# Kernel tuning notes

Hardware: AMD Instinct MI355X
Metric: run time of the kernel (lower is better)

## Reference

```python
import jax, jax.numpy as jnp
import numpy as np

B, N, M, K, D, DO = 4, 32768, 8192, 16, 128, 128


def setup_inputs() -> dict:
    key = jax.random.key(0)
    ks = jax.random.split(key, 8)
    return dict(
        xyz=jax.random.normal(ks[0], (B, N, 3), jnp.float32),
        x=jax.random.normal(ks[1], (B, D, N), jnp.float32),
        xyz_center=jax.random.normal(ks[2], (B, M, 3), jnp.float32),
        idx=jax.random.randint(ks[3], (B, M, K), 0, N, jnp.int32),
        alpha=jnp.ones((1,), jnp.float32),
        beta=jnp.ones((1,), jnp.float32),
        norm_radius=jnp.ones((1,), jnp.float32),
        w1=jax.random.normal(ks[4], (K, 3), jnp.float32) * 0.1,
        g1=jnp.ones((K,), jnp.float32),
        b1=jnp.zeros((K,), jnp.float32),
        w2=jax.random.normal(ks[5], (K, 2 * K), jnp.float32) * 0.1,
        g2=jnp.ones((K,), jnp.float32),
        b2=jnp.zeros((K,), jnp.float32),
        w3=jax.random.normal(ks[6], (K, 2 * K), jnp.float32) * 0.1,
        cv_w=jax.random.normal(ks[7], (DO, D, K), jnp.float32) * 0.02,
    )


def _inorm(t, g, b, eps=1e-5):
    # InstanceNorm2d: normalize each (batch, channel) plane over spatial dims (m, k)
    mu = t.mean(axis=(2, 3), keepdims=True)
    var = t.var(axis=(2, 3), keepdims=True)
    return (t - mu) * jax.lax.rsqrt(var + eps) * g[None, :, None, None] + b[None, :, None, None]


def reference(xyz, x, xyz_center, idx, alpha, beta, norm_radius, w1, g1, b1, w2, g2, b2, w3, cv_w):
    k = idx.shape[-1]
    gather = jax.vmap(lambda pts, i: pts[i])  # per-batch gather
    xyz_group = gather(xyz, idx)                      # b m k 3
    x_group = gather(jnp.swapaxes(x, 1, 2), idx)      # b m k d

    pts = xyz_group - xyz_center[:, :, None, :]       # b m k 3
    # dist computed on detached pts (torch .detach())
    dist = jnp.sqrt(jnp.sum(jnp.square(jax.lax.stop_gradient(pts)), -1))  # b m k
    mean_radius = dist.max(-1).mean()
    nr = norm_radius * 0.9 + mean_radius * 0.1        # EMA-updated radius (non-trainable)
    pts = pts / nr

    dw = jax.nn.sigmoid(-alpha * dist + beta)         # b m k
    s = dw.sum(-1, keepdims=True)
    s = s + (s == 0).astype(dw.dtype) + 1e-6
    dw = dw / s * k
    dw4 = dw[:, None, :, :]                           # b 1 m k

    ptsT = jnp.transpose(pts, (0, 3, 1, 2))           # b 3 m k
    mat = jax.nn.relu(_inorm(jnp.einsum('bcmk,oc->bomk', ptsT, w1), g1, b1))
    mp1 = jnp.broadcast_to((mat * dw4).max(-1, keepdims=True), mat.shape)
    mat = jax.nn.relu(_inorm(jnp.einsum('bcmk,oc->bomk', jnp.concatenate([mat, mp1], 1), w2), g2, b2))
    mp2 = jnp.broadcast_to((mat * dw4).max(-1, keepdims=True), mat.shape)
    mat = jax.nn.relu(jnp.einsum('bcmk,oc->bomk', jnp.concatenate([mat, mp2], 1), w3)) * dw4

    out = jnp.einsum('bmkd,bjmk->bdmj', x_group, mat)  # b d m k
    out = jnp.einsum('bdmj,odj->bom', out, cv_w)
    return out
```

## Files before the change

### kernel.cpp

```cpp
#include <hip/hip_runtime.h>
#include <hip/hip_bf16.h>

#define BB 4
#define NN 32768
#define MM 8192
#define KK 16
#define DD 128
#define DOUT 128
#define TT 2048

typedef unsigned short ushortT;
typedef unsigned int uintT;
typedef __attribute__((ext_vector_type(8))) short short8;
typedef __attribute__((ext_vector_type(4))) float f32x4;
typedef __attribute__((ext_vector_type(2))) float f32x2;

__device__ __forceinline__ ushortT f2bf(float f) {
  union { float f; uintT u; } v; v.f = f;
  uintT u = v.u;
  return (ushortT)((u + 0x7FFFu + ((u >> 16) & 1u)) >> 16);
}

#define ST_MAXD 0
#define ST_E1 16
#define ST_A1 160
#define ST_B1 224
#define ST_E2 288
#define ST_A2 416
#define ST_B2 480

__global__ __launch_bounds__(256) void kxT(const float* __restrict__ x, ushortT* __restrict__ xTb) {
  __shared__ float tile[32][33];
  const int b = blockIdx.z;
  const int n0 = blockIdx.x * 32, d0 = blockIdx.y * 32;
  const int tx = threadIdx.x, ty = threadIdx.y;
  const float* xp = x + (size_t)b * DD * NN;
  #pragma unroll
  for (int i = 0; i < 4; i++)
    tile[ty + i * 8][tx] = xp[(size_t)(d0 + ty + i * 8) * NN + n0 + tx];
  __syncthreads();
  ushortT* op = xTb + (size_t)b * NN * DD;
  #pragma unroll
  for (int i = 0; i < 4; i++)
    op[(size_t)(n0 + ty + i * 8) * DD + d0 + tx] = f2bf(tile[tx][ty + i * 8]);
}

__global__ __launch_bounds__(256) void kWb(const float* __restrict__ cw, ushortT* __restrict__ wb) {
  const int i = blockIdx.x * 256 + threadIdx.x;
  wb[i] = f2bf(cw[i]);
}

__global__ __launch_bounds__(256) void kpassA(const float* __restrict__ xyz,
    const float* __restrict__ xyzc, const int* __restrict__ idx,
    const float* __restrict__ w1, float* __restrict__ st, float4* __restrict__ pts4) {
  const int b = blockIdx.y;
  const int tid = threadIdx.x;
  const int mloc = tid >> 4, k = tid & 15;
  const int m = blockIdx.x * 16 + mloc;
  const int gi = (b * MM + m) * KK + k;
  const int n = idx[gi];
  const float cx = xyzc[(b * MM + m) * 3 + 0];
  const float cy = xyzc[(b * MM + m) * 3 + 1];
  const float cz = xyzc[(b * MM + m) * 3 + 2];
  const float* p = xyz + ((size_t)b * NN + n) * 3;
  const float px = p[0] - cx, py = p[1] - cy, pz = p[2] - cz;
  const float dist = sqrtf(px * px + py * py + pz * pz);
  pts4[gi] = (float4){px, py, pz, dist};
  float maxd = dist;
  maxd = fmaxf(maxd, __shfl_xor(maxd, 1));
  maxd = fmaxf(maxd, __shfl_xor(maxd, 2));
  maxd = fmaxf(maxd, __shfl_xor(maxd, 4));
  maxd = fmaxf(maxd, __shfl_xor(maxd, 8));
  __shared__ float red[16];
  __shared__ float wred[4][32];
  if (k == 0) red[mloc] = maxd;
  float vs[16], vq[16];
  #pragma unroll
  for (int o = 0; o < 16; o++) {
    float e = px * w1[3 * o] + py * w1[3 * o + 1] + pz * w1[3 * o + 2];
    vs[o] = e; vq[o] = e * e;
  }
  #pragma unroll
  for (int s = 1; s < 64; s <<= 1) {
    #pragma unroll
    for (int o = 0; o < 16; o++) {
      vs[o] += __shfl_xor(vs[o], s);
      vq[o] += __shfl_xor(vq[o], s);
    }
  }
  const int wv = tid >> 6, lane = tid & 63;
  if (lane == 0) {
    #pragma unroll
    for (int o = 0; o < 16; o++) { wred[wv][o] = vs[o]; wred[wv][16 + o] = vq[o]; }
  }
  __syncthreads();
  if (tid < 32) {
    float a = wred[0][tid] + wred[1][tid] + wred[2][tid] + wred[3][tid];
    atomicAdd(&st[ST_E1 + b * 32 + tid], a);
  }
  if (tid == 0) {
    float s = 0.f;
    #pragma unroll
    for (int i = 0; i < 16; i++) s += red[i];
    atomicAdd(&st[ST_MAXD], s);
  }
}

__global__ void kS1(const float* __restrict__ nrad, const float* __restrict__ g1,
                    const float* __restrict__ b1, float* __restrict__ st) {
  const int tid = threadIdx.x;
  if (tid >= 64) return;
  const float meanrad = st[ST_MAXD] / (float)(BB * MM);
  const float nr = nrad[0] * 0.9f + meanrad * 0.1f;
  const int b = tid >> 4, o = tid & 15;
  const float cnt = (float)(MM * KK);
  const float sum = st[ST_E1 + b * 32 + o];
  const float sq  = st[ST_E1 + b * 32 + 16 + o];
  const float mu = sum / cnt;
  float var = sq / cnt - mu * mu; var = fmaxf(var, 0.f);
  const float invs = rsqrtf(var + 1e-5f * nr * nr);
  const float a = invs * g1[o];
  st[ST_A1 + b * 16 + o] = a;
  st[ST_B1 + b * 16 + o] = b1[o] - mu * a;
}

__global__ __launch_bounds__(256) void kpassB(const float4* __restrict__ pts4,
    const float* __restrict__ alpha, const float* __restrict__ beta,
    const float* __restrict__ w1, const float* __restrict__ w2,
    float* __restrict__ st) {
  const int b = blockIdx.y;
  const int tid = threadIdx.x;
  __shared__ float w2s[512];
  __shared__ float wred[4][32];
  w2s[tid] = w2[tid]; w2s[256 + tid] = w2[256 + tid];
  const int gi = b * MM * KK + blockIdx.x * 256 + tid;
  const float4 p4 = pts4[gi];
  const float px = p4.x, py = p4.y, pz = p4.z, dist = p4.w;
  float dwv = 1.f / (1.f + expf(alpha[0] * dist - beta[0]));
  float s = dwv;
  s += __shfl_xor(s, 1); s += __shfl_xor(s, 2); s += __shfl_xor(s, 4); s += __shfl_xor(s, 8);
  s = s + (s == 0.f ? 1.f : 0.f) + 1e-6f;
  dwv = dwv / s * 16.f;
  float mat1[16], mp1[16];
  #pragma unroll
  for (int o = 0; o < 16; o++) {
    float e = px * w1[3 * o] + py * w1[3 * o + 1] + pz * w1[3 * o + 2];
    float v = e * st[ST_A1 + b * 16 + o] + st[ST_B1 + b * 16 + o];
    mat1[o] = fmaxf(v, 0.f);
    float t = mat1[o] * dwv;
    t = fmaxf(t, __shfl_xor(t, 1)); t = fmaxf(t, __shfl_xor(t, 2));
    t = fmaxf(t, __shfl_xor(t, 4)); t = fmaxf(t, __shfl_xor(t, 8));
    mp1[o] = t;
  }
  __syncthreads();
  float vs[16], vq[16];
  #pragma unroll
  for (int o = 0; o < 16; o++) {
    float acc = 0.f;
    #pragma unroll
    for (int c = 0; c < 16; c++)
      acc += mat1[c] * w2s[o * 32 + c] + mp1[c] * w2s[o * 32 + 16 + c];
    vs[o] = acc; vq[o] = acc * acc;
  }
  #pragma unroll
  for (int s2 = 1; s2 < 64; s2 <<= 1) {
    #pragma unroll
    for (int o = 0; o < 16; o++) {
      vs[o] += __shfl_xor(vs[o], s2);
      vq[o] += __shfl_xor(vq[o], s2);
    }
  }
  const int wv = tid >> 6, lane = tid & 63;
  if (lane == 0) {
    #pragma unroll
    for (int o = 0; o < 16; o++) { wred[wv][o] = vs[o]; wred[wv][16 + o] = vq[o]; }
  }
  __syncthreads();
  if (tid < 32) {
    float a = wred[0][tid] + wred[1][tid] + wred[2][tid] + wred[3][tid];
    atomicAdd(&st[ST_E2 + b * 32 + tid], a);
  }
}

__global__ void kS2(const float* __restrict__ g2, const float* __restrict__ b2,
                    float* __restrict__ st) {
  const int tid = threadIdx.x;
  if (tid >= 64) return;
  const int b = tid >> 4, o = tid & 15;
  const float cnt = (float)(MM * KK);
  const float sum = st[ST_E2 + b * 32 + o];
  const float sq  = st[ST_E2 + b * 32 + 16 + o];
  const float mu = sum / cnt;
  float var = sq / cnt - mu * mu; var = fmaxf(var, 0.f);
  const float invs = rsqrtf(var + 1e-5f);
  const float a = invs * g2[o];
  st[ST_A2 + b * 16 + o] = a;
  st[ST_B2 + b * 16 + o] = b2[o] - mu * a;
}

__global__ __launch_bounds__(512, 4) void kF1(const float4* __restrict__ pts4,
    const int* __restrict__ idx,
    const float* __restrict__ alpha, const float* __restrict__ beta,
    const float* __restrict__ w1, const float* __restrict__ w2, const float* __restrict__ w3,
    const float* __restrict__ st, const ushortT* __restrict__ xTb, ushortT* __restrict__ Aout) {
  __shared__ float w2s[512], w3s[512];
  __shared__ float mat3s[32 * 256];
  __shared__ ushortT nls[512];
  const int b = blockIdx.y;
  const int tid = threadIdx.x;
  const int m0 = blockIdx.x * 32;
  w2s[tid] = w2[tid];
  w3s[tid] = w3[tid];

  const int mloc = tid >> 4, k1 = tid & 15;
  const int gi = (b * MM + m0) * KK + tid;
  nls[tid] = (ushortT)idx[gi];
  const float4 p4 = pts4[gi];
  const float px = p4.x, py = p4.y, pz = p4.z, dist = p4.w;
  float dwv = 1.f / (1.f + expf(alpha[0] * dist - beta[0]));
  {
    float s = dwv;
    s += __shfl_xor(s, 1); s += __shfl_xor(s, 2); s += __shfl_xor(s, 4); s += __shfl_xor(s, 8);
    s = s + (s == 0.f ? 1.f : 0.f) + 1e-6f;
    dwv = dwv / s * 16.f;
  }
  float mat1[16], mp1[16];
  #pragma unroll
  for (int o = 0; o < 16; o++) {
    float e = px * w1[3 * o] + py * w1[3 * o + 1] + pz * w1[3 * o + 2];
    float v = e * st[ST_A1 + b * 16 + o] + st[ST_B1 + b * 16 + o];
    mat1[o] = fmaxf(v, 0.f);
    float t = mat1[o] * dwv;
    t = fmaxf(t, __shfl_xor(t, 1)); t = fmaxf(t, __shfl_xor(t, 2));
    t = fmaxf(t, __shfl_xor(t, 4)); t = fmaxf(t, __shfl_xor(t, 8));
    mp1[o] = t;
  }
  __syncthreads();
  {
    float mat2[16], mp2[16];
    #pragma unroll
    for (int o = 0; o < 16; o++) {
      float acc = 0.f;
      #pragma unroll
      for (int c = 0; c < 16; c++)
        acc += mat1[c] * w2s[o * 32 + c] + mp1[c] * w2s[o * 32 + 16 + c];
      float v = acc * st[ST_A2 + b * 16 + o] + st[ST_B2 + b * 16 + o];
      mat2[o] = fmaxf(v, 0.f);
      float t = mat2[o] * dwv;
      t = fmaxf(t, __shfl_xor(t, 1)); t = fmaxf(t, __shfl_xor(t, 2));
      t = fmaxf(t, __shfl_xor(t, 4)); t = fmaxf(t, __shfl_xor(t, 8));
      mp2[o] = t;
    }
    const int swz1 = (k1 ^ (k1 >> 2)) & 3;
    float* m3w = &mat3s[mloc * 256 + k1 * 16];
    float m3v[16];
    #pragma unroll
    for (int j = 0; j < 16; j++) {
      float acc = 0.f;
      #pragma unroll
      for (int c = 0; c < 16; c++)
        acc += mat2[c] * w3s[j * 32 + c] + mp2[c] * w3s[j * 32 + 16 + c];
      m3v[j] = fmaxf(acc, 0.f) * dwv;
    }
    #pragma unroll
    for (int q = 0; q < 4; q++)
      *(f32x4*)(m3w + ((q ^ swz1) << 2)) =
          (f32x4){m3v[4 * q], m3v[4 * q + 1], m3v[4 * q + 2], m3v[4 * q + 3]};
  }
  __syncthreads();

  const int wid = tid >> 6;
  const int lane = tid & 63;
  const int jh = lane >> 5;
  const int dq = lane & 31;
  const int d0 = dq * 4;
  const int jq0 = jh * 2;
  const ushortT* xb = xTb + (size_t)b * NN * DD + d0;

  uint2 xA[16], xB[16];

#define PREF(dst, gg) do {                                                 \
    const ushortT* nb = &nls[((gg) * 8 + wid) * 16];                       \
    _Pragma("unroll")                                                      \
    for (int k = 0; k < 16; k++) {                                         \
      const uintT nn = nb[k];                                              \
      (dst)[k] = *(const uint2*)(xb + ((size_t)nn << 7));                  \
    }                                                                      \
  } while (0)

#define COMP(src, gg) do {                                                 \
    const int ml = (gg) * 8 + wid;                                         \
    const float* m3base = &mat3s[ml * 256];                                \
    f32x2 a2[4][4];                                                        \
    _Pragma("unroll")                                                      \
    for (int d = 0; d < 4; d++)                                            \
      _Pragma("unroll")                                                    \
      for (int c = 0; c < 4; c++) a2[d][c] = (f32x2){0.f, 0.f};            \
    _Pragma("unroll")                                                      \
    for (int k = 0; k < 16; k++) {                                         \
      const int sw = (k ^ (k >> 2)) & 3;                                   \
      const uint2 xv = (src)[k];                                           \
      const f32x4 mq0 = *(const f32x4*)(m3base + k * 16 + ((jq0 ^ sw) << 2));        \
      const f32x4 mq1 = *(const f32x4*)(m3base + k * 16 + (((jq0 + 1) ^ sw) << 2));  \
      float xs[4];                                                         \
      xs[0] = __uint_as_float(xv.x << 16);                                 \
      xs[1] = __uint_as_float(xv.x & 0xFFFF0000u);                         \
      xs[2] = __uint_as_float(xv.y << 16);                                 \
      xs[3] = __uint_as_float(xv.y & 0xFFFF0000u);                         \
      f32x2 mp[4];                                                         \
      mp[0] = mq0.lo; mp[1] = mq0.hi;                                      \
      mp[2] = mq1.lo; mp[3] = mq1.hi;                                      \
      _Pragma("unroll")                                                    \
      for (int d = 0; d < 4; d++) {                                        \
        const float xd = xs[d];                                            \
        _Pragma("unroll")                                                  \
        for (int c = 0; c < 4; c++)                                        \
          a2[d][c] += mp[c] * xd;                                          \
      }                                                                    \
    }                                                                      \
    ushortT* aop = Aout + ((size_t)b * MM + m0 + ml) * TT + d0 * 16 + jh * 8;  \
    _Pragma("unroll")                                                      \
    for (int d = 0; d < 4; d++) {                                          \
      uintT u[4];                                                          \
      _Pragma("unroll")                                                    \
      for (int c = 0; c < 4; c++)                                          \
        u[c] = (uintT)f2bf(a2[d][c].x) | ((uintT)f2bf(a2[d][c].y) << 16);  \
      *(uint4*)(aop + d * 16) = (uint4){u[0], u[1], u[2], u[3]};           \
    }                                                                      \
  } while (0)

  PREF(xA, 0);
  PREF(xB, 1);
  COMP(xA, 0);
  PREF(xA, 2);
  COMP(xB, 1);
  PREF(xB, 3);
  COMP(xA, 2);
  COMP(xB, 3);

#undef PREF
#undef COMP
}

__global__ __launch_bounds__(512) void kgemm(const ushortT* __restrict__ Wb,
                                             const ushortT* __restrict__ Aout,
                                             float* __restrict__ out) {
  __shared__ ushortT At[128 * 40];
  __shared__ ushortT Bt[128 * 40];
  const int b = blockIdx.y;
  const int m0 = blockIdx.x * 128;
  const int tid = threadIdx.x;
  const int w = tid >> 6, l = tid & 63;
  const int ow = (w >> 2) * 64, mw = (w & 3) * 32;
  const int fr = l & 15, fg = l >> 4;
  f32x4 acc[4][2];
  #pragma unroll
  for (int i = 0; i < 4; i++)
    #pragma unroll
    for (int j = 0; j < 2; j++)
      acc[i][j] = (f32x4){0.f, 0.f, 0.f, 0.f};
  const int srow = tid >> 2, sk = (tid & 3) * 8;
  const ushortT* wp = Wb + srow * TT + sk;
  const ushortT* ap = Aout + ((size_t)b * MM + m0 + srow) * TT + sk;
  for (int k0 = 0; k0 < TT; k0 += 32) {
    uint4 wv = *(const uint4*)(wp + k0);
    uint4 av = *(const uint4*)(ap + k0);
    *(uint4*)&At[srow * 40 + sk] = wv;
    *(uint4*)&Bt[srow * 40 + sk] = av;
    __syncthreads();
    short8 a[4], bfrag[2];
    #pragma unroll
    for (int i = 0; i < 4; i++) a[i] = *(short8*)&At[(ow + i * 16 + fr) * 40 + fg * 8];
    #pragma unroll
    for (int j = 0; j < 2; j++) bfrag[j] = *(short8*)&Bt[(mw + j * 16 + fr) * 40 + fg * 8];
    #pragma unroll
    for (int i = 0; i < 4; i++)
      #pragma unroll
      for (int j = 0; j < 2; j++)
        acc[i][j] = __builtin_amdgcn_mfma_f32_16x16x32_bf16(a[i], bfrag[j], acc[i][j], 0, 0, 0);
    __syncthreads();
  }
  #pragma unroll
  for (int i = 0; i < 4; i++)
    #pragma unroll
    for (int j = 0; j < 2; j++)
      #pragma unroll
      for (int r = 0; r < 4; r++) {
        const int o = ow + i * 16 + fg * 4 + r;
        const int m = m0 + mw + j * 16 + fr;
        out[((size_t)b * DOUT + o) * MM + m] = acc[i][j][r];
      }
}

#define XTB_OFF 0
#define PTS_OFF 33554432
#define AOUT_OFF 67108864
#define WB_OFF 201326592
#define ST_OFF 201850880

extern "C" void kernel_launch(void* const* d_in, const int* in_sizes, int n_in,
                              void* d_out, int out_size, void* d_ws, size_t ws_size,
                              hipStream_t stream) {
  const float* xyz  = (const float*)d_in[0];
  const float* x    = (const float*)d_in[1];
  const float* xyzc = (const float*)d_in[2];
  const int*   idx  = (const int*)d_in[3];
  const float* alpha = (const float*)d_in[4];
  const float* beta  = (const float*)d_in[5];
  const float* nrad  = (const float*)d_in[6];
  const float* w1 = (const float*)d_in[7];
  const float* g1 = (const float*)d_in[8];
  const float* b1 = (const float*)d_in[9];
  const float* w2 = (const float*)d_in[10];
  const float* g2 = (const float*)d_in[11];
  const float* b2 = (const float*)d_in[12];
  const float* w3 = (const float*)d_in[13];
  const float* cvw = (const float*)d_in[14];
  char* ws = (char*)d_ws;
  ushortT* xTb  = (ushortT*)(ws + XTB_OFF);
  float4*  pts4 = (float4*)(ws + PTS_OFF);
  ushortT* Aout = (ushortT*)(ws + AOUT_OFF);
  ushortT* Wb   = (ushortT*)(ws + WB_OFF);
  float*   st   = (float*)(ws + ST_OFF);
  float* out = (float*)d_out;

  hipMemsetAsync(st, 0, 4096, stream);
  kxT<<<dim3(NN / 32, DD / 32, BB), dim3(32, 8), 0, stream>>>(x, xTb);
  kWb<<<dim3(DOUT * TT / 256), 256, 0, stream>>>(cvw, Wb);
  kpassA<<<dim3(MM / 16, BB), 256, 0, stream>>>(xyz, xyzc, idx, w1, st, pts4);
  kS1<<<1, 64, 0, stream>>>(nrad, g1, b1, st);
  kpassB<<<dim3(MM / 16, BB), 256, 0, stream>>>(pts4, alpha, beta, w1, w2, st);
  kS2<<<1, 64, 0, stream>>>(g2, b2, st);
  kF1<<<dim3(MM / 32, BB), 512, 0, stream>>>(pts4, idx, alpha, beta, w1, w2, w3, st, xTb, Aout);
  kgemm<<<dim3(MM / 128, BB), 512, 0, stream>>>(Wb, Aout, out);
}
```

Baseline: 216.9 us.

## Overlap first neighbor gather with MLP compute and pack weights for paired FMAs

Issues the first batch of neighbor feature gathers before the layer-2/3 point MLP runs, so global-memory latency hides behind that arithmetic. Weights are stored in shared memory as transposed float pairs, letting the MLP use packed two-wide FMAs with broadcast shared-memory reads. Neighbor indices now come straight from global memory instead of a shared-memory staging copy, and the wave id is made uniform with readfirstlane. The early prefetch keeps 16 more uint2 registers live across the MLP, which raises register pressure and may cut occupancy.

```diff
diff --git a/kernel.cpp b/kernel.cpp
--- a/kernel.cpp
+++ b/kernel.cpp
@@ -203,18 +203,23 @@
     const float* __restrict__ alpha, const float* __restrict__ beta,
     const float* __restrict__ w1, const float* __restrict__ w2, const float* __restrict__ w3,
     const float* __restrict__ st, const ushortT* __restrict__ xTb, ushortT* __restrict__ Aout) {
-  __shared__ float w2s[512], w3s[512];
+  __shared__ f32x2 w2p[256], w3p[256];
   __shared__ float mat3s[32 * 256];
-  __shared__ ushortT nls[512];
   const int b = blockIdx.y;
   const int tid = threadIdx.x;
   const int m0 = blockIdx.x * 32;
-  w2s[tid] = w2[tid];
-  w3s[tid] = w3[tid];
+
+  {
+    const int t = tid & 255;
+    const int c = t >> 3, op = t & 7;
+    const float* wsrc = (tid < 256) ? w2 : w3;
+    f32x2 pr = {wsrc[(2 * op) * 32 + c], wsrc[(2 * op + 1) * 32 + c]};
+    if (tid < 256) w2p[c * 8 + op] = pr;
+    else           w3p[c * 8 + op] = pr;
+  }
 
   const int mloc = tid >> 4, k1 = tid & 15;
   const int gi = (b * MM + m0) * KK + tid;
-  nls[tid] = (ushortT)idx[gi];
   const float4 p4 = pts4[gi];
   const float px = p4.x, py = p4.y, pz = p4.z, dist = p4.w;
   float dwv = 1.f / (1.f + expf(alpha[0] * dist - beta[0]));
@@ -224,52 +229,21 @@
     s = s + (s == 0.f ? 1.f : 0.f) + 1e-6f;
     dwv = dwv / s * 16.f;
   }
-  float mat1[16], mp1[16];
+  float in1[32];
   #pragma unroll
   for (int o = 0; o < 16; o++) {
     float e = px * w1[3 * o] + py * w1[3 * o + 1] + pz * w1[3 * o + 2];
     float v = e * st[ST_A1 + b * 16 + o] + st[ST_B1 + b * 16 + o];
-    mat1[o] = fmaxf(v, 0.f);
-    float t = mat1[o] * dwv;
+    v = fmaxf(v, 0.f);
+    in1[o] = v;
+    float t = v * dwv;
     t = fmaxf(t, __shfl_xor(t, 1)); t = fmaxf(t, __shfl_xor(t, 2));
     t = fmaxf(t, __shfl_xor(t, 4)); t = fmaxf(t, __shfl_xor(t, 8));
-    mp1[o] = t;
-  }
-  __syncthreads();
-  {
-    float mat2[16], mp2[16];
-    #pragma unroll
-    for (int o = 0; o < 16; o++) {
-      float acc = 0.f;
-      #pragma unroll
-      for (int c = 0; c < 16; c++)
-        acc += mat1[c] * w2s[o * 32 + c] + mp1[c] * w2s[o * 32 + 16 + c];
-      float v = acc * st[ST_A2 + b * 16 + o] + st[ST_B2 + b * 16 + o];
-      mat2[o] = fmaxf(v, 0.f);
-      float t = mat2[o] * dwv;
-      t = fmaxf(t, __shfl_xor(t, 1)); t = fmaxf(t, __shfl_xor(t, 2));
-      t = fmaxf(t, __shfl_xor(t, 4)); t = fmaxf(t, __shfl_xor(t, 8));
-      mp2[o] = t;
-    }
-    const int swz1 = (k1 ^ (k1 >> 2)) & 3;
-    float* m3w = &mat3s[mloc * 256 + k1 * 16];
-    float m3v[16];
-    #pragma unroll
-    for (int j = 0; j < 16; j++) {
-      float acc = 0.f;
-      #pragma unroll
-      for (int c = 0; c < 16; c++)
-        acc += mat2[c] * w3s[j * 32 + c] + mp2[c] * w3s[j * 32 + 16 + c];
-      m3v[j] = fmaxf(acc, 0.f) * dwv;
-    }
-    #pragma unroll
-    for (int q = 0; q < 4; q++)
-      *(f32x4*)(m3w + ((q ^ swz1) << 2)) =
-          (f32x4){m3v[4 * q], m3v[4 * q + 1], m3v[4 * q + 2], m3v[4 * q + 3]};
-  }
-  __syncthreads();
-
-  const int wid = tid >> 6;
+    in1[16 + o] = t;
+  }
+  __syncthreads();
+
+  const int wid = __builtin_amdgcn_readfirstlane(tid >> 6);
   const int lane = tid & 63;
   const int jh = lane >> 5;
   const int dq = lane & 31;
@@ -280,13 +254,65 @@
   uint2 xA[16], xB[16];
 
 #define PREF(dst, gg) do {                                                 \
-    const ushortT* nb = &nls[((gg) * 8 + wid) * 16];                       \
+    const int* ib = idx + (((b * MM + m0 + (gg) * 8 + wid)) << 4);         \
     _Pragma("unroll")                                                      \
     for (int k = 0; k < 16; k++) {                                         \
-      const uintT nn = nb[k];                                              \
+      const uintT nn = (uintT)ib[k];                                       \
       (dst)[k] = *(const uint2*)(xb + ((size_t)nn << 7));                  \
     }                                                                      \
   } while (0)
+
+  PREF(xA, 0);
+
+  {
+    f32x2 acc2[8];
+    #pragma unroll
+    for (int op = 0; op < 8; op++) acc2[op] = (f32x2){0.f, 0.f};
+    #pragma unroll
+    for (int c = 0; c < 32; c++) {
+      const float s1 = in1[c];
+      #pragma unroll
+      for (int op = 0; op < 8; op++) acc2[op] += w2p[c * 8 + op] * s1;
+    }
+    float in2[32];
+    #pragma unroll
+    for (int op = 0; op < 8; op++) {
+      const int o0 = 2 * op, o1 = 2 * op + 1;
+      float v0 = acc2[op].x * st[ST_A2 + b * 16 + o0] + st[ST_B2 + b * 16 + o0];
+      float v1 = acc2[op].y * st[ST_A2 + b * 16 + o1] + st[ST_B2 + b * 16 + o1];
+      in2[o0] = fmaxf(v0, 0.f);
+      in2[o1] = fmaxf(v1, 0.f);
+    }
+    #pragma unroll
+    for (int o = 0; o < 16; o++) {
+      float t = in2[o] * dwv;
+      t = fmaxf(t, __shfl_xor(t, 1)); t = fmaxf(t, __shfl_xor(t, 2));
+      t = fmaxf(t, __shfl_xor(t, 4)); t = fmaxf(t, __shfl_xor(t, 8));
+      in2[16 + o] = t;
+    }
+    f32x2 acc3[8];
+    #pragma unroll
+    for (int op = 0; op < 8; op++) acc3[op] = (f32x2){0.f, 0.f};
+    #pragma unroll
+    for (int c = 0; c < 32; c++) {
+      const float s2 = in2[c];
+      #pragma unroll
+      for (int op = 0; op < 8; op++) acc3[op] += w3p[c * 8 + op] * s2;
+    }
+    float m3v[16];
+    #pragma unroll
+    for (int op = 0; op < 8; op++) {
+      m3v[2 * op]     = fmaxf(acc3[op].x, 0.f) * dwv;
+      m3v[2 * op + 1] = fmaxf(acc3[op].y, 0.f) * dwv;
+    }
+    const int swz1 = (k1 ^ (k1 >> 2)) & 3;
+    float* m3w = &mat3s[mloc * 256 + k1 * 16];
+    #pragma unroll
+    for (int q = 0; q < 4; q++)
+      *(f32x4*)(m3w + ((q ^ swz1) << 2)) =
+          (f32x4){m3v[4 * q], m3v[4 * q + 1], m3v[4 * q + 2], m3v[4 * q + 3]};
+  }
+  __syncthreads();
 
 #define COMP(src, gg) do {                                                 \
     const int ml = (gg) * 8 + wid;                                         \
@@ -329,7 +355,6 @@
     }                                                                      \
   } while (0)
 
-  PREF(xA, 0);
   PREF(xB, 1);
   COMP(xA, 0);
   PREF(xA, 2);
```

Measured after the change: 213.0 us. No clear change (-1.8%).

## Overlap first neighbor gather with MLP compute and drop shared-memory staging

Applied to the files above, without the earlier changes.

Moves the first prefetch of gathered x rows ahead of the layer-2/3 MLP so global gather latency overlaps the per-point arithmetic. Removes the w2/w3 and neighbor-index shared-memory staging and one barrier, reading weights as packed float2 uniform loads and indices directly from global memory. Packs the MLP activations into float2 vectors so the compiler can use packed FMA, and makes the wave id scalar. This raises register pressure (16 prefetched uint2 held live during the MLP) and repeats index loads from global memory.

```diff
diff --git a/kernel.cpp b/kernel.cpp
--- a/kernel.cpp
+++ b/kernel.cpp
@@ -203,18 +203,13 @@
     const float* __restrict__ alpha, const float* __restrict__ beta,
     const float* __restrict__ w1, const float* __restrict__ w2, const float* __restrict__ w3,
     const float* __restrict__ st, const ushortT* __restrict__ xTb, ushortT* __restrict__ Aout) {
-  __shared__ float w2s[512], w3s[512];
   __shared__ float mat3s[32 * 256];
-  __shared__ ushortT nls[512];
   const int b = blockIdx.y;
   const int tid = threadIdx.x;
   const int m0 = blockIdx.x * 32;
-  w2s[tid] = w2[tid];
-  w3s[tid] = w3[tid];
 
   const int mloc = tid >> 4, k1 = tid & 15;
   const int gi = (b * MM + m0) * KK + tid;
-  nls[tid] = (ushortT)idx[gi];
   const float4 p4 = pts4[gi];
   const float px = p4.x, py = p4.y, pz = p4.z, dist = p4.w;
   float dwv = 1.f / (1.f + expf(alpha[0] * dist - beta[0]));
@@ -224,52 +219,21 @@
     s = s + (s == 0.f ? 1.f : 0.f) + 1e-6f;
     dwv = dwv / s * 16.f;
   }
-  float mat1[16], mp1[16];
+
+  f32x2 v1[16];
   #pragma unroll
   for (int o = 0; o < 16; o++) {
     float e = px * w1[3 * o] + py * w1[3 * o + 1] + pz * w1[3 * o + 2];
     float v = e * st[ST_A1 + b * 16 + o] + st[ST_B1 + b * 16 + o];
-    mat1[o] = fmaxf(v, 0.f);
-    float t = mat1[o] * dwv;
+    v = fmaxf(v, 0.f);
+    float t = v * dwv;
     t = fmaxf(t, __shfl_xor(t, 1)); t = fmaxf(t, __shfl_xor(t, 2));
     t = fmaxf(t, __shfl_xor(t, 4)); t = fmaxf(t, __shfl_xor(t, 8));
-    mp1[o] = t;
-  }
-  __syncthreads();
-  {
-    float mat2[16], mp2[16];
-    #pragma unroll
-    for (int o = 0; o < 16; o++) {
-      float acc = 0.f;
-      #pragma unroll
-      for (int c = 0; c < 16; c++)
-        acc += mat1[c] * w2s[o * 32 + c] + mp1[c] * w2s[o * 32 + 16 + c];
-      float v = acc * st[ST_A2 + b * 16 + o] + st[ST_B2 + b * 16 + o];
-      mat2[o] = fmaxf(v, 0.f);
-      float t = mat2[o] * dwv;
-      t = fmaxf(t, __shfl_xor(t, 1)); t = fmaxf(t, __shfl_xor(t, 2));
-      t = fmaxf(t, __shfl_xor(t, 4)); t = fmaxf(t, __shfl_xor(t, 8));
-      mp2[o] = t;
-    }
-    const int swz1 = (k1 ^ (k1 >> 2)) & 3;
-    float* m3w = &mat3s[mloc * 256 + k1 * 16];
-    float m3v[16];
-    #pragma unroll
-    for (int j = 0; j < 16; j++) {
-      float acc = 0.f;
-      #pragma unroll
-      for (int c = 0; c < 16; c++)
-        acc += mat2[c] * w3s[j * 32 + c] + mp2[c] * w3s[j * 32 + 16 + c];
-      m3v[j] = fmaxf(acc, 0.f) * dwv;
-    }
-    #pragma unroll
-    for (int q = 0; q < 4; q++)
-      *(f32x4*)(m3w + ((q ^ swz1) << 2)) =
-          (f32x4){m3v[4 * q], m3v[4 * q + 1], m3v[4 * q + 2], m3v[4 * q + 3]};
-  }
-  __syncthreads();
-
-  const int wid = tid >> 6;
+    if (o & 1) { v1[o >> 1].y = v; v1[8 + (o >> 1)].y = t; }
+    else       { v1[o >> 1].x = v; v1[8 + (o >> 1)].x = t; }
+  }
+
+  const int wid = __builtin_amdgcn_readfirstlane(tid >> 6);
   const int lane = tid & 63;
   const int jh = lane >> 5;
   const int dq = lane & 31;
@@ -280,13 +244,57 @@
   uint2 xA[16], xB[16];
 
 #define PREF(dst, gg) do {                                                 \
-    const ushortT* nb = &nls[((gg) * 8 + wid) * 16];                       \
+    const int* ib = idx + (((b * MM + m0 + (gg) * 8 + wid)) << 4);         \
     _Pragma("unroll")                                                      \
     for (int k = 0; k < 16; k++) {                                         \
-      const uintT nn = nb[k];                                              \
+      const uintT nn = (uintT)ib[k];                                       \
       (dst)[k] = *(const uint2*)(xb + ((size_t)nn << 7));                  \
     }                                                                      \
   } while (0)
+
+  PREF(xA, 0);
+
+  {
+    float in2[16];
+    #pragma unroll
+    for (int o = 0; o < 16; o++) {
+      f32x2 acc = {0.f, 0.f};
+      #pragma unroll
+      for (int cp = 0; cp < 16; cp++) {
+        const f32x2 wv = *(const f32x2*)(w2 + o * 32 + 2 * cp);
+        acc += v1[cp] * wv;
+      }
+      float v = (acc.x + acc.y) * st[ST_A2 + b * 16 + o] + st[ST_B2 + b * 16 + o];
+      in2[o] = fmaxf(v, 0.f);
+    }
+    f32x2 v2[16];
+    #pragma unroll
+    for (int o = 0; o < 16; o++) {
+      float t = in2[o] * dwv;
+      t = fmaxf(t, __shfl_xor(t, 1)); t = fmaxf(t, __shfl_xor(t, 2));
+      t = fmaxf(t, __shfl_xor(t, 4)); t = fmaxf(t, __shfl_xor(t, 8));
+      if (o & 1) { v2[o >> 1].y = in2[o]; v2[8 + (o >> 1)].y = t; }
+      else       { v2[o >> 1].x = in2[o]; v2[8 + (o >> 1)].x = t; }
+    }
+    float m3v[16];
+    #pragma unroll
+    for (int j = 0; j < 16; j++) {
+      f32x2 acc = {0.f, 0.f};
+      #pragma unroll
+      for (int cp = 0; cp < 16; cp++) {
+        const f32x2 wv = *(const f32x2*)(w3 + j * 32 + 2 * cp);
+        acc += v2[cp] * wv;
+      }
+      m3v[j] = fmaxf(acc.x + acc.y, 0.f) * dwv;
+    }
+    const int swz1 = (k1 ^ (k1 >> 2)) & 3;
+    float* m3w = &mat3s[mloc * 256 + k1 * 16];
+    #pragma unroll
+    for (int q = 0; q < 4; q++)
+      *(f32x4*)(m3w + ((q ^ swz1) << 2)) =
+          (f32x4){m3v[4 * q], m3v[4 * q + 1], m3v[4 * q + 2], m3v[4 * q + 3]};
+  }
+  __syncthreads();
 
 #define COMP(src, gg) do {                                                 \
     const int ml = (gg) * 8 + wid;                                         \
@@ -329,7 +337,6 @@
     }                                                                      \
   } while (0)
 
-  PREF(xA, 0);
   PREF(xB, 1);
   COMP(xA, 0);
   PREF(xA, 2);
```

New measurement: 211.6 us (median of 2 runs). 1.03x faster.
